# Optimization experiments

Measured on AMD Instinct MI355X. Metric: run time of the kernel, lower is better.

## Reference

```python
import jax, jax.numpy as jnp
import numpy as np
from jax import lax

LBDA = 0.1
EPS = 0.01
NUM_CLASSES = 20


def setup_inputs() -> dict:
    key = jax.random.key(0)
    k1, k2 = jax.random.split(key)
    target_features = jax.random.normal(k1, (2048, 8, 2048), dtype=jnp.float32)
    support_features = jax.random.normal(k2, (100, 8, 2048), dtype=jnp.float32)
    # 20-way 5-shot: every class present so per-class mean is well defined
    support_labels = jnp.repeat(jnp.arange(NUM_CLASSES, dtype=jnp.int32), 100 // NUM_CLASSES)
    return {
        "target_features": target_features,
        "support_features": support_features,
        "support_labels": support_labels,
    }


def _softmin(xs, lbda):
    # -lbda * log(sum_i exp(-x_i/lbda)), stable
    return -lbda * jax.nn.logsumexp(jnp.stack([-x / lbda for x in xs], axis=0), axis=0)


def otam_cum_dist(dists, lbda=LBDA):
    # dists: [Q, Sp, L, S] frame distance matrices
    d = jnp.pad(dists, ((0, 0), (0, 0), (0, 0), (1, 1)))  # pad columns -> M = S + 2
    M = d.shape[-1]
    # row 0: running sum along columns (cum[0,0] = d[0,0] = 0 from padding)
    row0 = jnp.cumsum(d[:, :, 0, :], axis=-1)

    def step(prev_row, d_row):
        # prev_row, d_row: [Q, Sp, M]; column 0 is never written -> stays 0
        cur = [jnp.zeros_like(d_row[..., 0])]
        cur.append(d_row[..., 1] + _softmin([prev_row[..., 0], prev_row[..., 1], cur[0]], lbda))
        for m in range(2, M - 1):
            cur.append(d_row[..., m] + _softmin([prev_row[..., m - 1], cur[m - 1]], lbda))
        cur.append(d_row[..., M - 1] + _softmin([prev_row[..., M - 2], prev_row[..., M - 1], cur[M - 2]], lbda))
        new_row = jnp.stack(cur, axis=-1)
        return new_row, None

    d_rows = jnp.moveaxis(d[:, :, 1:, :], 2, 0)  # [L-1, Q, Sp, M]
    final_row, _ = lax.scan(step, row0, d_rows)
    return final_row[..., -1]  # [Q, Sp]


def cos_sim(x, y, eps=EPS):
    num = x @ y.T
    den = jnp.linalg.norm(x, axis=-1)[:, None] * jnp.linalg.norm(y, axis=-1)[None, :] + eps
    return num / den


def reference(target_features, support_features, support_labels):
    Q, S, D = target_features.shape
    Sp = support_features.shape[0]
    tf = target_features.reshape(Q * S, D)
    sf = support_features.reshape(Sp * S, D)
    frame_dists = 1.0 - cos_sim(tf, sf)  # [Q*S, Sp*S]
    # '(tb ts) (sb ss) -> tb sb ts ss'
    dists = frame_dists.reshape(Q, S, Sp, S).transpose(0, 2, 1, 3)
    cum_dists = otam_cum_dist(dists) + otam_cum_dist(dists.transpose(0, 1, 3, 2))  # [Q, Sp]
    # per-class mean over support (torch.unique returns sorted labels 0..C-1)
    onehot = (support_labels[:, None] == jnp.arange(NUM_CLASSES)[None, :]).astype(cum_dists.dtype)
    onehot = onehot / jnp.sum(onehot, axis=0, keepdims=True)
    class_dists = cum_dists @ onehot  # [Q, C]
    return -class_dists[None]  # logits [1, Q, C]
```

## Files before the change

kernel.cpp:

```cpp
#include <hip/hip_runtime.h>

#define QN    2048
#define SS    8
#define DD    2048
#define SP    100
#define NCLS  20
#define MROWS (QN*SS)
#define NROWS (SP*SS)
#define NPAD  896
#define KK    DD
#define MT    64
#define NT    128

typedef __bf16 bf16x8 __attribute__((ext_vector_type(8)));
typedef float  f32x4  __attribute__((ext_vector_type(4)));

__device__ __forceinline__ unsigned short f2bf(float f) {
    unsigned int u = __float_as_uint(f);
    u += 0x7fffu + ((u >> 16) & 1u);
    return (unsigned short)(u >> 16);
}

__global__ void cvt_kernel(const float* __restrict__ tf, const float* __restrict__ sf,
                           unsigned short* __restrict__ Abf, unsigned short* __restrict__ Bbf,
                           float* __restrict__ nA, float* __restrict__ nB)
{
    int row = blockIdx.x;
    int tid = threadIdx.x;
    const float* src = nullptr;
    unsigned short* dst;
    float* nrm; int r;
    if (row < MROWS) { src = tf + (size_t)row * DD; dst = Abf + (size_t)row * DD; nrm = nA; r = row; }
    else {
        r = row - MROWS;
        dst = Bbf + (size_t)r * DD; nrm = nB;
        if (r < NROWS) src = sf + (size_t)r * DD;
    }
    float s = 0.f;
    union { uint4 u; unsigned short h[8]; } pk;
    if (src) {
        float4 v0 = *(const float4*)(src + tid * 8);
        float4 v1 = *(const float4*)(src + tid * 8 + 4);
        s = v0.x*v0.x + v0.y*v0.y + v0.z*v0.z + v0.w*v0.w
          + v1.x*v1.x + v1.y*v1.y + v1.z*v1.z + v1.w*v1.w;
        pk.h[0]=f2bf(v0.x); pk.h[1]=f2bf(v0.y); pk.h[2]=f2bf(v0.z); pk.h[3]=f2bf(v0.w);
        pk.h[4]=f2bf(v1.x); pk.h[5]=f2bf(v1.y); pk.h[6]=f2bf(v1.z); pk.h[7]=f2bf(v1.w);
    } else {
        pk.u = make_uint4(0, 0, 0, 0);
    }
    *(uint4*)(dst + (size_t)tid * 8) = pk.u;

    for (int o = 32; o; o >>= 1) s += __shfl_down(s, o);
    __shared__ float red[4];
    if ((tid & 63) == 0) red[tid >> 6] = s;
    __syncthreads();
    if (tid == 0) nrm[r] = sqrtf(red[0] + red[1] + red[2] + red[3]);
}

__device__ __forceinline__ float softmin2(float a, float b) {
    float mn = fminf(a, b), mx = fmaxf(a, b);
    return mn - 0.1f * __logf(1.0f + __expf((mn - mx) * 10.0f));
}
__device__ __forceinline__ float softmin3(float a, float b, float c) {
    float mn = fminf(fminf(a, b), c);
    float sum = __expf((mn - a) * 10.0f) + __expf((mn - b) * 10.0f) + __expf((mn - c) * 10.0f);
    return mn - 0.1f * __logf(sum);
}

__device__ __forceinline__ void gld16(const void* g, void* l) {
    __builtin_amdgcn_global_load_lds(
        (const __attribute__((address_space(1))) unsigned int*)g,
        (__attribute__((address_space(3))) unsigned int*)l, 16, 0, 0);
}

__device__ __forceinline__ float cellf(const uint4* raw, int a, int b) {
    const unsigned* p = (const unsigned*)raw;
    unsigned wv = p[a * 4 + (b >> 1)];
    return __uint_as_float((b & 1) ? (wv & 0xffff0000u) : (wv << 16));
}

#define EBS (32 * 72)

__global__ __launch_bounds__(256, 4) void gemm_kernel(
    const unsigned short* __restrict__ A,
    const unsigned short* __restrict__ B,
    const float* __restrict__ nA, const float* __restrict__ nB,
    float* __restrict__ cum)
{
    __shared__ __align__(16) unsigned short smem[4 * EBS];
    unsigned short* Als = smem;
    unsigned short* Bls = smem + MT * 32;

    const int mt  = blockIdx.x;
    const int nt  = blockIdx.y;
    const int tid = threadIdx.x;
    const int lane = tid & 63;
    const int w    = tid >> 6;
    const int wm   = (w & 1) * 32, wn = (w >> 1) * 64;
    const int col  = lane & 15, kg = lane >> 4;

    f32x4 acc[2][4] = {};

    const int rr = tid >> 2, ks = (tid & 3) * 8;
    const unsigned short* Ap  = A + (size_t)(mt * MT  + rr) * KK + ks;
    const unsigned short* Bp0 = B + (size_t)(nt * NT  + rr) * KK + ks;
    const unsigned short* Bp1 = B + (size_t)(nt * NT + 64 + rr) * KK + ks;

    for (int kk = 0; kk < KK; kk += 32) {
        __syncthreads();
        gld16(Ap  + kk, (char*)Als + tid * 16);
        gld16(Bp0 + kk, (char*)Bls + tid * 16);
        gld16(Bp1 + kk, (char*)Bls + (tid + 256) * 16);
        __syncthreads();
        bf16x8 af[2], bfr[4];
#pragma unroll
        for (int i = 0; i < 2; i++) af[i]  = *(const bf16x8*)(Als + (wm + i * 16 + col) * 32 + kg * 8);
#pragma unroll
        for (int i = 0; i < 4; i++) bfr[i] = *(const bf16x8*)(Bls + (wn + i * 16 + col) * 32 + kg * 8);
#pragma unroll
        for (int mi = 0; mi < 2; mi++)
#pragma unroll
            for (int ni = 0; ni < 4; ni++)
                acc[mi][ni] = __builtin_amdgcn_mfma_f32_16x16x32_bf16(af[mi], bfr[ni], acc[mi][ni], 0, 0, 0);
    }

    __syncthreads();

    unsigned short* eb = smem + w * EBS;
    const int mbase = mt * MT + wm;
    const int nbase = nt * NT + wn;

#pragma unroll
    for (int mi = 0; mi < 2; mi++) {
        float nx[4];
#pragma unroll
        for (int r = 0; r < 4; r++) nx[r] = nA[mbase + mi * 16 + kg * 4 + r];
#pragma unroll
        for (int ni = 0; ni < 4; ni++) {
            const float ny = nB[nbase + ni * 16 + col];
#pragma unroll
            for (int r = 0; r < 4; r++) {
                float d = 1.0f - acc[mi][ni][r] / (nx[r] * ny + 0.01f);
                eb[(mi * 16 + kg * 4 + r) * 72 + ni * 16 + col] = f2bf(d);
            }
        }
    }

    const int pr  = lane & 31;
    const int qv2 = pr >> 3, sv = pr & 7;
    const int dir = lane >> 5;

    uint4 raw[8];
    const unsigned short* tb = eb + (qv2 * 8) * 72 + sv * 8;
#pragma unroll
    for (int l = 0; l < 8; l++) raw[l] = *(const uint4*)(tb + l * 72);

    float prev[10], cur[10];
    prev[0] = 0.f;
#pragma unroll
    for (int m = 1; m <= 8; m++) {
        float v0 = cellf(raw, 0, m - 1), v1 = cellf(raw, m - 1, 0);
        prev[m] = prev[m - 1] + (dir ? v1 : v0);
    }
    prev[9] = prev[8];
#pragma unroll
    for (int l = 1; l < 8; l++) {
        float d[8];
#pragma unroll
        for (int j = 0; j < 8; j++) {
            float v0 = cellf(raw, l, j), v1 = cellf(raw, j, l);
            d[j] = dir ? v1 : v0;
        }
        cur[1] = d[0] + softmin3(prev[0], prev[1], 0.0f);
#pragma unroll
        for (int m = 2; m <= 8; m++)
            cur[m] = d[m - 1] + softmin2(prev[m - 1], cur[m - 1]);
        cur[9] = softmin3(prev[8], prev[9], cur[8]);
#pragma unroll
        for (int m = 1; m < 10; m++) prev[m] = cur[m];
    }
    float res = prev[9];
    res += __shfl_down(res, 32);
    if (dir == 0) {
        const int qg = mt * 8 + (wm >> 3) + qv2;
        const int sg = nt * 16 + (wn >> 3) + sv;
        if (sg < SP) cum[(size_t)qg * SP + sg] = res;
    }
}

__global__ void cls_kernel(const float* __restrict__ cum, const int* __restrict__ labels,
                           float* __restrict__ out)
{
    int idx = blockIdx.x * 256 + threadIdx.x;
    int q = idx / NCLS, c = idx % NCLS;
    float s = 0.f; int n = 0;
    const float* row = cum + (size_t)q * SP;
    for (int sp = 0; sp < SP; sp++) {
        if (labels[sp] == c) { s += row[sp]; n++; }
    }
    out[idx] = -s / (float)n;
}

extern "C" void kernel_launch(void* const* d_in, const int* in_sizes, int n_in,
                              void* d_out, int out_size, void* d_ws, size_t ws_size,
                              hipStream_t stream)
{
    const float* tf     = (const float*)d_in[0];
    const float* sf     = (const float*)d_in[1];
    const int*   labels = (const int*)d_in[2];
    float* out = (float*)d_out;

    char* ws = (char*)d_ws;
    const size_t szA    = (size_t)MROWS * KK * 2;
    const size_t szB    = (size_t)NPAD  * KK * 2;
    const size_t szNA   = (size_t)MROWS * 4;
    const size_t szNB   = (size_t)NPAD  * 4;
    unsigned short* Abf = (unsigned short*)ws;
    unsigned short* Bbf = (unsigned short*)(ws + szA);
    float* nA   = (float*)(ws + szA + szB);
    float* nB   = (float*)(ws + szA + szB + szNA);
    float* cum  = (float*)(ws + szA + szB + szNA + szNB);

    cvt_kernel<<<MROWS + NPAD, 256, 0, stream>>>(tf, sf, Abf, Bbf, nA, nB);
    gemm_kernel<<<dim3(MROWS / MT, NPAD / NT), 256, 0, stream>>>(Abf, Bbf, nA, nB, cum);
    cls_kernel<<<160, 256, 0, stream>>>(cum, labels, out);
}
```

Before: 322.2 us.

## Enlarge GEMM tile to 128x128 with BK=64 and k-major LDS layout

The GEMM block tile grows from 64x128 to 128x128 with a K step of 64, and each wave now computes a 64x64 sub-tile (4x4 MFMAs). Shared memory is laid out k-group-major so each fragment read is a contiguous 8-element slice, and the OTAM epilogue runs in two passes to reuse the per-wave staging buffer. The conversion kernel also switches to coalesced stride-4 loads and stores. The aim is higher arithmetic intensity per LDS load and fewer barriers per unit of work, at the cost of more registers, lower occupancy (launch bounds 2) and fewer blocks.

```diff
diff --git a/kernel.cpp b/kernel.cpp
--- a/kernel.cpp
+++ b/kernel.cpp
@@ -9,8 +9,7 @@
 #define NROWS (SP*SS)
 #define NPAD  896
 #define KK    DD
-#define MT    64
-#define NT    128
+#define BK    64
 
 typedef __bf16 bf16x8 __attribute__((ext_vector_type(8)));
 typedef float  f32x4  __attribute__((ext_vector_type(4)));
@@ -37,18 +36,17 @@
         if (r < NROWS) src = sf + (size_t)r * DD;
     }
     float s = 0.f;
-    union { uint4 u; unsigned short h[8]; } pk;
+    ushort4 p0 = make_ushort4(0,0,0,0), p1 = p0;
     if (src) {
-        float4 v0 = *(const float4*)(src + tid * 8);
-        float4 v1 = *(const float4*)(src + tid * 8 + 4);
+        float4 v0 = *(const float4*)(src + tid * 4);
+        float4 v1 = *(const float4*)(src + 1024 + tid * 4);
         s = v0.x*v0.x + v0.y*v0.y + v0.z*v0.z + v0.w*v0.w
           + v1.x*v1.x + v1.y*v1.y + v1.z*v1.z + v1.w*v1.w;
-        pk.h[0]=f2bf(v0.x); pk.h[1]=f2bf(v0.y); pk.h[2]=f2bf(v0.z); pk.h[3]=f2bf(v0.w);
-        pk.h[4]=f2bf(v1.x); pk.h[5]=f2bf(v1.y); pk.h[6]=f2bf(v1.z); pk.h[7]=f2bf(v1.w);
-    } else {
-        pk.u = make_uint4(0, 0, 0, 0);
-    }
-    *(uint4*)(dst + (size_t)tid * 8) = pk.u;
+        p0 = make_ushort4(f2bf(v0.x), f2bf(v0.y), f2bf(v0.z), f2bf(v0.w));
+        p1 = make_ushort4(f2bf(v1.x), f2bf(v1.y), f2bf(v1.z), f2bf(v1.w));
+    }
+    *(ushort4*)(dst + tid * 4)        = p0;
+    *(ushort4*)(dst + 1024 + tid * 4) = p1;
 
     for (int o = 32; o; o >>= 1) s += __shfl_down(s, o);
     __shared__ float red[4];
@@ -81,110 +79,124 @@
 
 #define EBS (32 * 72)
 
-__global__ __launch_bounds__(256, 4) void gemm_kernel(
+__global__ __launch_bounds__(256, 2) void gemm_kernel(
     const unsigned short* __restrict__ A,
     const unsigned short* __restrict__ B,
     const float* __restrict__ nA, const float* __restrict__ nB,
     float* __restrict__ cum)
 {
-    __shared__ __align__(16) unsigned short smem[4 * EBS];
+    __shared__ __align__(16) unsigned short smem[16384];
     unsigned short* Als = smem;
-    unsigned short* Bls = smem + MT * 32;
+    unsigned short* Bls = smem + 8192;
 
     const int mt  = blockIdx.x;
     const int nt  = blockIdx.y;
     const int tid = threadIdx.x;
     const int lane = tid & 63;
     const int w    = tid >> 6;
-    const int wm   = (w & 1) * 32, wn = (w >> 1) * 64;
+    const int wm   = (w & 1) * 64, wn = (w >> 1) * 64;
     const int col  = lane & 15, kg = lane >> 4;
 
-    f32x4 acc[2][4] = {};
-
-    const int rr = tid >> 2, ks = (tid & 3) * 8;
-    const unsigned short* Ap  = A + (size_t)(mt * MT  + rr) * KK + ks;
-    const unsigned short* Bp0 = B + (size_t)(nt * NT  + rr) * KK + ks;
-    const unsigned short* Bp1 = B + (size_t)(nt * NT + 64 + rr) * KK + ks;
-
-    for (int kk = 0; kk < KK; kk += 32) {
+    f32x4 acc[4][4] = {};
+
+    const unsigned short* Apt[4];
+    const unsigned short* Bpt[4];
+#pragma unroll
+    for (int j = 0; j < 4; j++) {
+        int s = j * 256 + tid;
+        Apt[j] = A + (size_t)(mt * 128 + (s & 127)) * KK + (s >> 7) * 8;
+        Bpt[j] = B + (size_t)(nt * 128 + (s & 127)) * KK + (s >> 7) * 8;
+    }
+
+    for (int kk = 0; kk < KK; kk += BK) {
         __syncthreads();
-        gld16(Ap  + kk, (char*)Als + tid * 16);
-        gld16(Bp0 + kk, (char*)Bls + tid * 16);
-        gld16(Bp1 + kk, (char*)Bls + (tid + 256) * 16);
+#pragma unroll
+        for (int j = 0; j < 4; j++) gld16(Apt[j] + kk, (char*)Als + (j * 256 + tid) * 16);
+#pragma unroll
+        for (int j = 0; j < 4; j++) gld16(Bpt[j] + kk, (char*)Bls + (j * 256 + tid) * 16);
         __syncthreads();
-        bf16x8 af[2], bfr[4];
-#pragma unroll
-        for (int i = 0; i < 2; i++) af[i]  = *(const bf16x8*)(Als + (wm + i * 16 + col) * 32 + kg * 8);
-#pragma unroll
-        for (int i = 0; i < 4; i++) bfr[i] = *(const bf16x8*)(Bls + (wn + i * 16 + col) * 32 + kg * 8);
-#pragma unroll
-        for (int mi = 0; mi < 2; mi++)
-#pragma unroll
-            for (int ni = 0; ni < 4; ni++)
-                acc[mi][ni] = __builtin_amdgcn_mfma_f32_16x16x32_bf16(af[mi], bfr[ni], acc[mi][ni], 0, 0, 0);
+#pragma unroll
+        for (int ks = 0; ks < 2; ks++) {
+            bf16x8 af[4], bfr[4];
+            const int ko = (ks * 4 + kg) * 1024;
+#pragma unroll
+            for (int i = 0; i < 4; i++) af[i]  = *(const bf16x8*)(Als + ko + (wm + i * 16 + col) * 8);
+#pragma unroll
+            for (int i = 0; i < 4; i++) bfr[i] = *(const bf16x8*)(Bls + ko + (wn + i * 16 + col) * 8);
+#pragma unroll
+            for (int mi = 0; mi < 4; mi++)
+#pragma unroll
+                for (int ni = 0; ni < 4; ni++)
+                    acc[mi][ni] = __builtin_amdgcn_mfma_f32_16x16x32_bf16(af[mi], bfr[ni], acc[mi][ni], 0, 0, 0);
+        }
     }
 
     __syncthreads();
 
     unsigned short* eb = smem + w * EBS;
-    const int mbase = mt * MT + wm;
-    const int nbase = nt * NT + wn;
-
-#pragma unroll
-    for (int mi = 0; mi < 2; mi++) {
-        float nx[4];
-#pragma unroll
-        for (int r = 0; r < 4; r++) nx[r] = nA[mbase + mi * 16 + kg * 4 + r];
-#pragma unroll
-        for (int ni = 0; ni < 4; ni++) {
-            const float ny = nB[nbase + ni * 16 + col];
-#pragma unroll
-            for (int r = 0; r < 4; r++) {
-                float d = 1.0f - acc[mi][ni][r] / (nx[r] * ny + 0.01f);
-                eb[(mi * 16 + kg * 4 + r) * 72 + ni * 16 + col] = f2bf(d);
-            }
-        }
-    }
-
+    const int mbase = mt * 128 + wm;
+    const int nbase = nt * 128 + wn;
     const int pr  = lane & 31;
     const int qv2 = pr >> 3, sv = pr & 7;
     const int dir = lane >> 5;
 
-    uint4 raw[8];
-    const unsigned short* tb = eb + (qv2 * 8) * 72 + sv * 8;
-#pragma unroll
-    for (int l = 0; l < 8; l++) raw[l] = *(const uint4*)(tb + l * 72);
-
-    float prev[10], cur[10];
-    prev[0] = 0.f;
-#pragma unroll
-    for (int m = 1; m <= 8; m++) {
-        float v0 = cellf(raw, 0, m - 1), v1 = cellf(raw, m - 1, 0);
-        prev[m] = prev[m - 1] + (dir ? v1 : v0);
-    }
-    prev[9] = prev[8];
-#pragma unroll
-    for (int l = 1; l < 8; l++) {
-        float d[8];
-#pragma unroll
-        for (int j = 0; j < 8; j++) {
-            float v0 = cellf(raw, l, j), v1 = cellf(raw, j, l);
-            d[j] = dir ? v1 : v0;
-        }
-        cur[1] = d[0] + softmin3(prev[0], prev[1], 0.0f);
-#pragma unroll
-        for (int m = 2; m <= 8; m++)
-            cur[m] = d[m - 1] + softmin2(prev[m - 1], cur[m - 1]);
-        cur[9] = softmin3(prev[8], prev[9], cur[8]);
-#pragma unroll
-        for (int m = 1; m < 10; m++) prev[m] = cur[m];
-    }
-    float res = prev[9];
-    res += __shfl_down(res, 32);
-    if (dir == 0) {
-        const int qg = mt * 8 + (wm >> 3) + qv2;
-        const int sg = nt * 16 + (wn >> 3) + sv;
-        if (sg < SP) cum[(size_t)qg * SP + sg] = res;
+#pragma unroll
+    for (int p = 0; p < 2; p++) {
+        if (p) __syncthreads();
+#pragma unroll
+        for (int mi2 = 0; mi2 < 2; mi2++) {
+            const int mi = p * 2 + mi2;
+            float nx[4];
+#pragma unroll
+            for (int r = 0; r < 4; r++) nx[r] = nA[mbase + mi * 16 + kg * 4 + r];
+#pragma unroll
+            for (int ni = 0; ni < 4; ni++) {
+                const float ny = nB[nbase + ni * 16 + col];
+#pragma unroll
+                for (int r = 0; r < 4; r++) {
+                    float d = 1.0f - acc[mi][ni][r] / (nx[r] * ny + 0.01f);
+                    eb[(mi2 * 16 + kg * 4 + r) * 72 + ni * 16 + col] = f2bf(d);
+                }
+            }
+        }
+        __syncthreads();
+
+        uint4 raw[8];
+        const unsigned short* tb = eb + (qv2 * 8) * 72 + sv * 8;
+#pragma unroll
+        for (int l = 0; l < 8; l++) raw[l] = *(const uint4*)(tb + l * 72);
+
+        float prev[10], cur[10];
+        prev[0] = 0.f;
+#pragma unroll
+        for (int m = 1; m <= 8; m++) {
+            float v0 = cellf(raw, 0, m - 1), v1 = cellf(raw, m - 1, 0);
+            prev[m] = prev[m - 1] + (dir ? v1 : v0);
+        }
+        prev[9] = prev[8];
+#pragma unroll
+        for (int l = 1; l < 8; l++) {
+            float d[8];
+#pragma unroll
+            for (int j = 0; j < 8; j++) {
+                float v0 = cellf(raw, l, j), v1 = cellf(raw, j, l);
+                d[j] = dir ? v1 : v0;
+            }
+            cur[1] = d[0] + softmin3(prev[0], prev[1], 0.0f);
+#pragma unroll
+            for (int m = 2; m <= 8; m++)
+                cur[m] = d[m - 1] + softmin2(prev[m - 1], cur[m - 1]);
+            cur[9] = softmin3(prev[8], prev[9], cur[8]);
+#pragma unroll
+            for (int m = 1; m < 10; m++) prev[m] = cur[m];
+        }
+        float res = prev[9];
+        res += __shfl_down(res, 32);
+        if (dir == 0) {
+            const int qg = mt * 16 + (wm >> 3) + p * 4 + qv2;
+            const int sg = nt * 16 + (wn >> 3) + sv;
+            if (sg < SP) cum[(size_t)qg * SP + sg] = res;
+        }
     }
 }
 
@@ -222,6 +234,6 @@
     float* cum  = (float*)(ws + szA + szB + szNA + szNB);
 
     cvt_kernel<<<MROWS + NPAD, 256, 0, stream>>>(tf, sf, Abf, Bbf, nA, nB);
-    gemm_kernel<<<dim3(MROWS / MT, NPAD / NT), 256, 0, stream>>>(Abf, Bbf, nA, nB, cum);
+    gemm_kernel<<<dim3(MROWS / 128, NPAD / 128), 256, 0, stream>>>(Abf, Bbf, nA, nB, cum);
     cls_kernel<<<160, 256, 0, stream>>>(cum, labels, out);
 }
```

Result: slower. 360.4 us (+11.9%).
